# Kernel optimization log

Measured on AMD Instinct MI355X. Metric: run time of the kernel, lower is better.

Reference implementation:

```python
import jax, jax.numpy as jnp
import numpy as np

N_HEAD = 16

def setup_inputs() -> dict:
    key = jax.random.key(0)
    k0, k1, k2, k3 = jax.random.split(key, 4)
    S, E, H, T = 2048, 1024, N_HEAD, 4096
    d = E // H
    return {
        "x": jax.random.normal(k0, (S, E), jnp.float32),
        "past": jax.random.normal(k1, (2, H, T, d), jnp.float32),  # stacked [pk, pv]
        "W1": jax.random.normal(k2, (E, 3 * E), jnp.float32) * 0.02,  # c_attn (Conv1D k=1 == linear)
        "b1": jnp.zeros((3 * E,), jnp.float32),
        "W2": jax.random.normal(k3, (E, E), jnp.float32) * 0.02,  # c_proj
        "b2": jnp.zeros((E,), jnp.float32),
        "past_length": 2048,
    }


def reference(x, past, W1, b1, W2, b2, past_length):
    H = N_HEAD
    S, E = x.shape
    d = E // H

    c = x @ W1 + b1  # [S, 3E]
    q, k, v = jnp.split(c, 3, axis=1)

    def split_heads(t):  # [S, E] -> [H, S, d]
        return jnp.transpose(t.reshape(S, H, d), (1, 0, 2))

    q, k, v = split_heads(q), split_heads(k), split_heads(v)

    pk, pv = past[0], past[1]  # [H, T, d]
    k = jax.lax.dynamic_update_slice_in_dim(pk, k, past_length, axis=1)
    v = jax.lax.dynamic_update_slice_in_dim(pv, v, past_length, axis=1)

    # attention scores [H, S, T]
    w = jnp.einsum('hid,hjd->hij', q, k) / np.sqrt(d)
    ns = k.shape[1]
    i = jnp.arange(S)[:, None]
    j = jnp.arange(ns)[None, :]
    b = (i >= j - past_length).astype(w.dtype)
    w = w * b - jnp.float32(1e10) * (1 - b)
    w = jax.nn.softmax(w, axis=-1)

    a = jnp.einsum('hij,hjd->hid', w, v)  # [H, S, d]
    # faithful to original: start index clamps to 0 since axis len == S
    a = jax.lax.dynamic_slice_in_dim(a, past_length, S, axis=1)
    a = jnp.transpose(a, (1, 0, 2)).reshape(S, E)  # merge heads

    out = a @ W2 + b2
    new_cache = jnp.stack([k, v], axis=0)
    return out, new_cache
```

## Files before the change

### kernel.cpp

```cpp
#include <hip/hip_runtime.h>
#include <hip/hip_bf16.h>
#include <stdint.h>


#define S_LEN 2048
#define E_DIM 1024
#define NHEAD 16
#define HDIM  64
#define T_LEN 4096
#define PASTL 2048

typedef __bf16 bf16x8 __attribute__((ext_vector_type(8)));
typedef __bf16 bf16x4 __attribute__((ext_vector_type(4)));
typedef float  f32x4  __attribute__((ext_vector_type(4)));

static __device__ __forceinline__ f32x4 mfma_bf16(bf16x8 a, bf16x8 b, f32x4 c) {
  return __builtin_amdgcn_mfma_f32_16x16x32_bf16(a, b, c, 0, 0, 0);
}

static __device__ __forceinline__ unsigned int f2bf(float f) {
  union { float f; unsigned int u; } v; v.f = f;
  unsigned int u = v.u;
  return (u + 0x7fffu + ((u >> 16) & 1u)) >> 16;
}

static __device__ __forceinline__ float bf2f(unsigned short u) {
  union { unsigned int u; float f; } v; v.u = (unsigned int)u << 16;
  return v.f;
}

#define GLOBAL_LOAD_LDS16(gptr, lptr)                                              \
  __builtin_amdgcn_global_load_lds(                                                \
      (const __attribute__((address_space(1))) unsigned int*)(gptr),               \
      (__attribute__((address_space(3))) unsigned int*)(lptr), 16, 0, 0)

__global__ __launch_bounds__(256) void prep_kernel(
    const float* __restrict__ past, const float* __restrict__ x,
    const float* __restrict__ W1, const float* __restrict__ W2,
    float* __restrict__ cache, unsigned short* __restrict__ kb,
    unsigned short* __restrict__ xb, unsigned short* __restrict__ w1t,
    unsigned short* __restrict__ w2t, unsigned short* __restrict__ vtb) {
  __shared__ float tile[64][65];
  const int bid = blockIdx.x;
  const int tid = threadIdx.x;
  const int tx = tid & 63, ty = tid >> 6;

  if (bid < 512) {
    const int h = bid >> 5;
    const int t0 = (bid & 31) * 64;
    const float* in = past + (size_t)(NHEAD + h) * T_LEN * HDIM;
    unsigned short* outp = vtb + (size_t)h * HDIM * T_LEN;
#pragma unroll
    for (int r = 0; r < 64; r += 4)
      tile[r + ty][tx] = in[(size_t)(t0 + r + ty) * HDIM + tx];
    __syncthreads();
#pragma unroll
    for (int r = 0; r < 64; r += 4)
      outp[(size_t)(r + ty) * T_LEN + t0 + tx] = f2bf(tile[tx][r + ty]);
  } else if (bid < 1536) {
    const float* in;
    unsigned short* outp;
    int rows, cols, c0, r0;
    if (bid < 1280) {
      int u = bid - 512;
      in = W1; outp = w1t; rows = 1024; cols = 3072;
      c0 = (u % 48) * 64; r0 = (u / 48) * 64;
    } else {
      int u = bid - 1280;
      in = W2; outp = w2t; rows = 1024; cols = 1024;
      c0 = (u & 15) * 64; r0 = (u >> 4) * 64;
    }
#pragma unroll
    for (int r = 0; r < 64; r += 4)
      tile[r + ty][tx] = in[(size_t)(r0 + r + ty) * cols + c0 + tx];
    __syncthreads();
#pragma unroll
    for (int r = 0; r < 64; r += 4)
      outp[(size_t)(c0 + r + ty) * rows + r0 + tx] = f2bf(tile[tx][r + ty]);
  } else {
    const int n4p = (2 * NHEAD * PASTL * HDIM) / 4;
    const int n4x = (S_LEN * E_DIM) / 4;
    for (int i = (bid - 1536) * 256 + tid; i < n4p + n4x; i += 2048 * 256) {
      if (i < n4p) {
        int e = i * 4;
        int d = e & 63;
        int t = (e >> 6) & (PASTL - 1);
        int hh = (e >> 17) & (NHEAD - 1);
        int kv = e >> 21;
        size_t full = (((size_t)kv * NHEAD + hh) * T_LEN + t) * HDIM + d;
        float4 v = *(const float4*)(past + full);
        *(float4*)(cache + full) = v;
        if (kv == 0) {
          ushort4 u;
          u.x = f2bf(v.x); u.y = f2bf(v.y); u.z = f2bf(v.z); u.w = f2bf(v.w);
          *(ushort4*)(kb + full) = u;
        }
      } else {
        int j = i - n4p;
        float4 v = ((const float4*)x)[j];
        ushort4 u;
        u.x = f2bf(v.x); u.y = f2bf(v.y); u.z = f2bf(v.z); u.w = f2bf(v.w);
        ((ushort4*)xb)[j] = u;
      }
    }
  }
}

template <int MODE>
__global__ __launch_bounds__(256) void gemm_bt_kernel(
    const unsigned short* __restrict__ A, const unsigned short* __restrict__ Bt,
    const float* __restrict__ bias, int K,
    float* __restrict__ out_f32, unsigned short* __restrict__ qb,
    float* __restrict__ cache_k, float* __restrict__ cache_v,
    unsigned short* __restrict__ kb, unsigned short* __restrict__ vtb) {
  __shared__ alignas(16) unsigned short As[2][64 * 64];
  __shared__ alignas(16) unsigned short Bs[2][128 * 64];
  const int NPX = (MODE == 0) ? 3 : 1;
  const int bid = blockIdx.x;
  const int xcd = bid & 7;
  const int loc = bid >> 3;
  const int n_idx = xcd * NPX + loc % NPX;
  const int m_idx = loc / NPX;
  const int m0 = m_idx * 64, n0 = n_idx * 128;

  const int tid = threadIdx.x;
  const int lane = tid & 63;
  const int w = tid >> 6;
  const int wm = w >> 1, wn = w & 1;
  const int lr = lane & 15;
  const int lg = lane >> 4;

  f32x4 acc[2][4];
#pragma unroll
  for (int i = 0; i < 2; ++i)
#pragma unroll
    for (int j = 0; j < 4; ++j) acc[i][j] = f32x4{0.f, 0.f, 0.f, 0.f};

  const int srow = tid >> 3;
  const int sseg = (tid & 7) ^ (srow & 7);
  const unsigned short* ga0 = A + (size_t)(m0 + srow) * K + sseg * 8;
  const unsigned short* gb0 = Bt + (size_t)(n0 + srow) * K + sseg * 8;

  auto stage = [&](int b, int k0) {
    GLOBAL_LOAD_LDS16(ga0 + k0, (char*)As[b] + tid * 16);
    GLOBAL_LOAD_LDS16(ga0 + (size_t)32 * K + k0, (char*)As[b] + 4096 + tid * 16);
#pragma unroll
    for (int j = 0; j < 4; ++j)
      GLOBAL_LOAD_LDS16(gb0 + (size_t)(32 * j) * K + k0,
                        (char*)Bs[b] + j * 4096 + tid * 16);
  };

  const int NKS = K >> 6;
  stage(0, 0);
  int cur = 0;
  for (int i = 0; i < NKS; ++i) {
    asm volatile("s_waitcnt vmcnt(0)" ::: "memory");
    __builtin_amdgcn_s_barrier();
    __builtin_amdgcn_sched_barrier(0);
    if (i + 1 < NKS) stage(cur ^ 1, (i + 1) * 64);

#pragma unroll
    for (int kk = 0; kk < 2; ++kk) {
      bf16x8 af[2], bfr[4];
#pragma unroll
      for (int mi = 0; mi < 2; ++mi) {
        int row = wm * 32 + mi * 16 + lr;
        int slot = (kk * 4 + lg) ^ (row & 7);
        af[mi] = *reinterpret_cast<const bf16x8*>((const char*)As[cur] + row * 128 + slot * 16);
      }
#pragma unroll
      for (int ni = 0; ni < 4; ++ni) {
        int row = wn * 64 + ni * 16 + lr;
        int slot = (kk * 4 + lg) ^ (row & 7);
        bfr[ni] = *reinterpret_cast<const bf16x8*>((const char*)Bs[cur] + row * 128 + slot * 16);
      }
#pragma unroll
      for (int mi = 0; mi < 2; ++mi)
#pragma unroll
        for (int ni = 0; ni < 4; ++ni)
          acc[mi][ni] = mfma_bf16(af[mi], bfr[ni], acc[mi][ni]);
    }
    cur ^= 1;
  }

#pragma unroll
  for (int ni = 0; ni < 4; ++ni) {
    int n = n0 + wn * 64 + ni * 16 + lr;
    float bv = bias[n];
#pragma unroll
    for (int mi = 0; mi < 2; ++mi) {
      int mbase = m0 + wm * 32 + mi * 16 + lg * 4;
      float v4[4];
#pragma unroll
      for (int r = 0; r < 4; ++r) v4[r] = acc[mi][ni][r] + bv;
      if (MODE == 0) {
        if (n < E_DIM) {
#pragma unroll
          for (int r = 0; r < 4; ++r)
            qb[(size_t)(mbase + r) * E_DIM + n] = f2bf(v4[r] * 0.18033688f);
        } else if (n < 2 * E_DIM) {
          int e = n - E_DIM;
          size_t base = ((size_t)(e >> 6) * T_LEN + (PASTL + mbase)) * HDIM + (e & 63);
#pragma unroll
          for (int r = 0; r < 4; ++r) {
            cache_k[base + (size_t)r * HDIM] = v4[r];
            kb[base + (size_t)r * HDIM] = f2bf(v4[r]);
          }
        } else {
          int e = n - 2 * E_DIM;
          int hh = e >> 6, d = e & 63;
          size_t base = ((size_t)hh * T_LEN + (PASTL + mbase)) * HDIM + d;
#pragma unroll
          for (int r = 0; r < 4; ++r) cache_v[base + (size_t)r * HDIM] = v4[r];
          ushort4 u;
          u.x = f2bf(v4[0]); u.y = f2bf(v4[1]);
          u.z = f2bf(v4[2]); u.w = f2bf(v4[3]);
          *(ushort4*)(vtb + ((size_t)hh * HDIM + d) * T_LEN + PASTL + mbase) = u;
        }
      } else {
#pragma unroll
        for (int r = 0; r < 4; ++r)
          out_f32[(size_t)(mbase + r) * E_DIM + n] = v4[r];
      }
    }
  }
}

__global__ __launch_bounds__(256) void attn_kernel(
    const unsigned short* __restrict__ qb, const unsigned short* __restrict__ kb,
    const unsigned short* __restrict__ vt,
    unsigned short* __restrict__ o_part, float* __restrict__ l_part) {
  __shared__ alignas(16) unsigned short Ks[2][64 * 64];
  __shared__ alignas(16) unsigned short Vs[2][64 * 64];
  __shared__ alignas(16) __bf16 p_lds[4][32][72];
  const int fid = blockIdx.x;
  const int h = (fid & 7) + ((fid >= 448) ? 8 : 0);
  const int g = (fid >> 3) - ((fid >= 448) ? 56 : 0);
  int x, c;
  if (g < 24) { x = g / 3; c = g - 3 * x; }
  else { int g2 = g - 24; x = 8 + (g2 >> 2); c = g2 & 3; }

  const int tid = threadIdx.x;
  const int w = tid >> 6;
  const int lane = tid & 63;
  const int lr = lane & 15;
  const int lg = lane >> 4;
  const int qb0 = x * 128;
  const int q0 = qb0 + w * 32;

  const unsigned short* qr0 = qb + (size_t)(q0 + lr) * E_DIM + h * HDIM + lg * 8;
  const unsigned short* qr1 = qb + (size_t)(q0 + 16 + lr) * E_DIM + h * HDIM + lg * 8;
  const bf16x8 qf00 = *reinterpret_cast<const bf16x8*>(qr0);
  const bf16x8 qf01 = *reinterpret_cast<const bf16x8*>(qr0 + 32);
  const bf16x8 qf10 = *reinterpret_cast<const bf16x8*>(qr1);
  const bf16x8 qf11 = *reinterpret_cast<const bf16x8*>(qr1 + 32);

  const unsigned short* kh = kb + (size_t)h * T_LEN * HDIM;
  const unsigned short* vh = vt + (size_t)h * HDIM * T_LEN;

  const int srow = tid >> 3;
  const int sseg = (tid & 7) ^ (srow & 7);
  const unsigned short* ksrc = kh + (size_t)srow * HDIM + sseg * 8;
  const unsigned short* vsrc = vh + (size_t)srow * T_LEN + sseg * 8;

  f32x4 o[2][4];
  float lsum[2][2];
#pragma unroll
  for (int sb = 0; sb < 2; ++sb) {
    lsum[sb][0] = lsum[sb][1] = 0.f;
#pragma unroll
    for (int jd = 0; jd < 4; ++jd) o[sb][jd] = f32x4{0.f, 0.f, 0.f, 0.f};
  }

  const int jmaxq = q0 + PASTL;
  const int NTfull = 34 + 2 * x;
  const int tb = c * 16;
  const int te = (tb + 16 < NTfull) ? tb + 16 : NTfull;
  const int NT = te - tb;
  const int tbeg = tb * 64;

  auto stageK = [&](int b, int t0) {
    GLOBAL_LOAD_LDS16(ksrc + (size_t)t0 * HDIM, (char*)Ks[b] + tid * 16);
    GLOBAL_LOAD_LDS16(ksrc + (size_t)(t0 + 32) * HDIM, (char*)Ks[b] + 4096 + tid * 16);
  };
  auto stageV = [&](int b, int t0) {
    GLOBAL_LOAD_LDS16(vsrc + t0, (char*)Vs[b] + tid * 16);
    GLOBAL_LOAD_LDS16(vsrc + t0 + (size_t)32 * T_LEN, (char*)Vs[b] + 4096 + tid * 16);
  };

  stageK(0, tbeg);
  stageV(0, tbeg);
  int cur = 0;
  int t0 = tbeg;
  for (int i = 0; i < NT; ++i, t0 += 64) {
    const bool more = (i + 1 < NT);
    asm volatile("s_waitcnt vmcnt(2)" ::: "memory");
    __builtin_amdgcn_s_barrier();
    __builtin_amdgcn_sched_barrier(0);
    if (more) stageK(cur ^ 1, t0 + 64);

    bf16x8 kf[4][2];
#pragma unroll
    for (int j = 0; j < 4; ++j) {
      int row = j * 16 + lr;
      int s0 = lg ^ (row & 7), s1 = (4 + lg) ^ (row & 7);
      kf[j][0] = *reinterpret_cast<const bf16x8*>((const char*)Ks[cur] + row * 128 + s0 * 16);
      kf[j][1] = *reinterpret_cast<const bf16x8*>((const char*)Ks[cur] + row * 128 + s1 * 16);
    }

    f32x4 sc[2][4];
#pragma unroll
    for (int sb = 0; sb < 2; ++sb)
#pragma unroll
      for (int j = 0; j < 4; ++j) sc[sb][j] = f32x4{0.f, 0.f, 0.f, 0.f};
    __builtin_amdgcn_s_setprio(1);
#pragma unroll
    for (int j = 0; j < 4; ++j) {
      sc[0][j] = mfma_bf16(kf[j][0], qf00, sc[0][j]);
      sc[0][j] = mfma_bf16(kf[j][1], qf01, sc[0][j]);
      sc[1][j] = mfma_bf16(kf[j][0], qf10, sc[1][j]);
      sc[1][j] = mfma_bf16(kf[j][1], qf11, sc[1][j]);
    }
    __builtin_amdgcn_s_setprio(0);

    const bool partial = (t0 + 63 > jmaxq);
    const int thr = q0 + PASTL - t0 + lr;
    const int lg4 = lg * 4;
#pragma unroll
    for (int sb = 0; sb < 2; ++sb) {
#pragma unroll
      for (int j = 0; j < 4; ++j) {
        bf16x4 pk;
#pragma unroll
        for (int r = 0; r < 4; ++r) {
          float p = __builtin_amdgcn_exp2f(sc[sb][j][r]);
          if (partial && (j * 16 + lg4 + r > thr + sb * 16)) p = 0.f;
          lsum[sb][r >> 1] += p;
          pk[r] = (__bf16)p;
        }
        *reinterpret_cast<bf16x4*>(&p_lds[w][sb * 16 + lr][j * 16 + lg4]) = pk;
      }
    }
    bf16x8 pa[2][2];
#pragma unroll
    for (int sb = 0; sb < 2; ++sb) {
      pa[sb][0] = *reinterpret_cast<const bf16x8*>(&p_lds[w][sb * 16 + lr][lg * 8]);
      pa[sb][1] = *reinterpret_cast<const bf16x8*>(&p_lds[w][sb * 16 + lr][32 + lg * 8]);
    }

    if (more) {
      asm volatile("s_waitcnt vmcnt(2)" ::: "memory");
    } else {
      asm volatile("s_waitcnt vmcnt(0)" ::: "memory");
    }
    __builtin_amdgcn_s_barrier();
    __builtin_amdgcn_sched_barrier(0);
    if (more) stageV(cur ^ 1, t0 + 64);

    __builtin_amdgcn_s_setprio(1);
#pragma unroll
    for (int jd = 0; jd < 4; ++jd) {
      int row = jd * 16 + lr;
      int s0 = lg ^ (row & 7), s1 = (4 + lg) ^ (row & 7);
      bf16x8 vf0 = *reinterpret_cast<const bf16x8*>((const char*)Vs[cur] + row * 128 + s0 * 16);
      bf16x8 vf1 = *reinterpret_cast<const bf16x8*>((const char*)Vs[cur] + row * 128 + s1 * 16);
      o[0][jd] = mfma_bf16(pa[0][0], vf0, o[0][jd]);
      o[0][jd] = mfma_bf16(pa[0][1], vf1, o[0][jd]);
      o[1][jd] = mfma_bf16(pa[1][0], vf0, o[1][jd]);
      o[1][jd] = mfma_bf16(pa[1][1], vf1, o[1][jd]);
    }
    __builtin_amdgcn_s_setprio(0);
    cur ^= 1;
  }

  unsigned short* op = o_part + ((size_t)(c * NHEAD + h) * S_LEN) * HDIM;
  float* lp = l_part + (size_t)(c * NHEAD + h) * S_LEN;
#pragma unroll
  for (int sb = 0; sb < 2; ++sb) {
    float ls = lsum[sb][0] + lsum[sb][1];
    ls += __shfl_xor(ls, 16);
    ls += __shfl_xor(ls, 32);
    if (lg == 0) lp[q0 + sb * 16 + lr] = ls;
#pragma unroll
    for (int jd = 0; jd < 4; ++jd) {
#pragma unroll
      for (int r = 0; r < 4; ++r) {
        int row = q0 + sb * 16 + lg * 4 + r;
        op[(size_t)row * HDIM + jd * 16 + lr] = f2bf(o[sb][jd][r]);
      }
    }
  }
}

__global__ __launch_bounds__(256) void attn_merge_kernel(
    const unsigned short* __restrict__ o_part, const float* __restrict__ l_part,
    unsigned short* __restrict__ ab) {
  const int flat = blockIdx.x * 256 + threadIdx.x;
  const int d4 = flat & 15;
  const int row = (flat >> 4) & (S_LEN - 1);
  const int h = flat >> 15;
  const int nc = (row < 1024) ? 3 : 4;
  const size_t cstride_o = (size_t)NHEAD * S_LEN * HDIM;
  const size_t base_o = (((size_t)h * S_LEN) + row) * HDIM + d4 * 4;
  float acc[4] = {0.f, 0.f, 0.f, 0.f};
  float l = 0.f;
  for (int cc = 0; cc < nc; ++cc) {
    ushort4 u = *(const ushort4*)(o_part + cc * cstride_o + base_o);
    acc[0] += bf2f(u.x); acc[1] += bf2f(u.y);
    acc[2] += bf2f(u.z); acc[3] += bf2f(u.w);
    l += l_part[(size_t)cc * NHEAD * S_LEN + (size_t)h * S_LEN + row];
  }
  float inv = 1.f / l;
  ushort4 u;
  u.x = f2bf(acc[0] * inv);
  u.y = f2bf(acc[1] * inv);
  u.z = f2bf(acc[2] * inv);
  u.w = f2bf(acc[3] * inv);
  *(ushort4*)(ab + (size_t)row * E_DIM + h * HDIM + d4 * 4) = u;
}


extern "C" void kernel_launch(void* const* d_in, const int* in_sizes, int n_in,
                              void* d_out, int out_size, void* d_ws, size_t ws_size,
                              hipStream_t stream) {
  (void)in_sizes; (void)n_in; (void)out_size; (void)ws_size;
  const float* x    = (const float*)d_in[0];
  const float* past = (const float*)d_in[1];
  const float* W1   = (const float*)d_in[2];
  const float* b1   = (const float*)d_in[3];
  const float* W2   = (const float*)d_in[4];
  const float* b2   = (const float*)d_in[5];

  float* out = (float*)d_out;
  float* cache_k = out + (size_t)S_LEN * E_DIM;
  float* cache_v = cache_k + (size_t)NHEAD * T_LEN * HDIM;

  char* ws = (char*)d_ws;
  unsigned short* w2t = (unsigned short*)(ws);
  unsigned short* qb  = (unsigned short*)(ws + (size_t)(2u  << 20));
  unsigned short* kb  = (unsigned short*)(ws + (size_t)(6u  << 20));
  unsigned short* vtb = (unsigned short*)(ws + (size_t)(14u << 20));
  unsigned short* xb  = (unsigned short*)(ws + (size_t)(22u << 20));
  unsigned short* ab  = (unsigned short*)(ws + (size_t)(22u << 20));
  unsigned short* w1t = (unsigned short*)(ws + (size_t)(26u << 20));
  unsigned short* o_part = (unsigned short*)(ws + (size_t)(26u << 20));
  float* l_part = (float*)(ws + (size_t)(42u << 20));

  prep_kernel<<<3584, 256, 0, stream>>>(past, x, W1, W2, cache_k, kb, xb, w1t,
                                        w2t, vtb);
  gemm_bt_kernel<0><<<768, 256, 0, stream>>>(
      xb, w1t, b1, 1024, nullptr, qb, cache_k, cache_v, kb, vtb);
  attn_kernel<<<dim3(896), 256, 0, stream>>>(qb, kb, vtb, o_part, l_part);
  attn_merge_kernel<<<(NHEAD * S_LEN * 16) / 256, 256, 0, stream>>>(o_part, l_part, ab);
  gemm_bt_kernel<1><<<256, 256, 0, stream>>>(
      ab, w2t, b2, 1024, out, nullptr, nullptr, nullptr, nullptr, nullptr);
}
```

Baseline: 118.5 us.

## Switch attention to 32x32x16 MFMA and pass P via permlane32 swaps instead of LDS

Rewrites the attention inner loop to use 32x32x16 bf16 MFMA tiles so the transposed score layout lines up with the PV operand layout. The probabilities are packed to bf16 pairs in registers and rearranged across half-waves with permlane32_swap, which removes the per-tile LDS round trip through p_lds. Unmasked tiles also get a branch-free exp path. This changes the register layout and the output write pattern, and the larger accumulators may add register pressure.

```diff
diff --git a/kernel.cpp b/kernel.cpp
--- a/kernel.cpp
+++ b/kernel.cpp
@@ -12,10 +12,16 @@
 
 typedef __bf16 bf16x8 __attribute__((ext_vector_type(8)));
 typedef __bf16 bf16x4 __attribute__((ext_vector_type(4)));
+typedef __bf16 bf16x2 __attribute__((ext_vector_type(2)));
 typedef float  f32x4  __attribute__((ext_vector_type(4)));
+typedef float  f32x16 __attribute__((ext_vector_type(16)));
+typedef unsigned u32x2 __attribute__((ext_vector_type(2)));
 
 static __device__ __forceinline__ f32x4 mfma_bf16(bf16x8 a, bf16x8 b, f32x4 c) {
   return __builtin_amdgcn_mfma_f32_16x16x32_bf16(a, b, c, 0, 0, 0);
+}
+static __device__ __forceinline__ f32x16 mfma32(bf16x8 a, bf16x8 b, f32x16 c) {
+  return __builtin_amdgcn_mfma_f32_32x32x16_bf16(a, b, c, 0, 0, 0);
 }
 
 static __device__ __forceinline__ unsigned int f2bf(float f) {
@@ -27,6 +33,11 @@
 static __device__ __forceinline__ float bf2f(unsigned short u) {
   union { unsigned int u; float f; } v; v.u = (unsigned int)u << 16;
   return v.f;
+}
+
+static __device__ __forceinline__ unsigned pkbf(float lo, float hi) {
+  bf16x2 t = {(__bf16)lo, (__bf16)hi};
+  return __builtin_bit_cast(unsigned, t);
 }
 
 #define GLOBAL_LOAD_LDS16(gptr, lptr)                                              \
@@ -232,7 +243,6 @@
     unsigned short* __restrict__ o_part, float* __restrict__ l_part) {
   __shared__ alignas(16) unsigned short Ks[2][64 * 64];
   __shared__ alignas(16) unsigned short Vs[2][64 * 64];
-  __shared__ alignas(16) __bf16 p_lds[4][32][72];
   const int fid = blockIdx.x;
   const int h = (fid & 7) + ((fid >= 448) ? 8 : 0);
   const int g = (fid >> 3) - ((fid >= 448) ? 56 : 0);
@@ -243,17 +253,16 @@
   const int tid = threadIdx.x;
   const int w = tid >> 6;
   const int lane = tid & 63;
-  const int lr = lane & 15;
-  const int lg = lane >> 4;
-  const int qb0 = x * 128;
-  const int q0 = qb0 + w * 32;
-
-  const unsigned short* qr0 = qb + (size_t)(q0 + lr) * E_DIM + h * HDIM + lg * 8;
-  const unsigned short* qr1 = qb + (size_t)(q0 + 16 + lr) * E_DIM + h * HDIM + lg * 8;
-  const bf16x8 qf00 = *reinterpret_cast<const bf16x8*>(qr0);
-  const bf16x8 qf01 = *reinterpret_cast<const bf16x8*>(qr0 + 32);
-  const bf16x8 qf10 = *reinterpret_cast<const bf16x8*>(qr1);
-  const bf16x8 qf11 = *reinterpret_cast<const bf16x8*>(qr1 + 32);
+  const int l31 = lane & 31;
+  const int hi = lane >> 5;
+  const int hi4 = hi * 4;
+  const int q0 = x * 128 + w * 32;
+
+  const unsigned short* qrow = qb + (size_t)(q0 + l31) * E_DIM + h * HDIM + hi * 8;
+  bf16x8 qf[4];
+#pragma unroll
+  for (int kk = 0; kk < 4; ++kk)
+    qf[kk] = *reinterpret_cast<const bf16x8*>(qrow + kk * 16);
 
   const unsigned short* kh = kb + (size_t)h * T_LEN * HDIM;
   const unsigned short* vh = vt + (size_t)h * HDIM * T_LEN;
@@ -263,21 +272,17 @@
   const unsigned short* ksrc = kh + (size_t)srow * HDIM + sseg * 8;
   const unsigned short* vsrc = vh + (size_t)srow * T_LEN + sseg * 8;
 
-  f32x4 o[2][4];
-  float lsum[2][2];
-#pragma unroll
-  for (int sb = 0; sb < 2; ++sb) {
-    lsum[sb][0] = lsum[sb][1] = 0.f;
-#pragma unroll
-    for (int jd = 0; jd < 4; ++jd) o[sb][jd] = f32x4{0.f, 0.f, 0.f, 0.f};
-  }
-
-  const int jmaxq = q0 + PASTL;
+  f32x16 o0, o1, zc;
+#pragma unroll
+  for (int i = 0; i < 16; ++i) { o0[i] = 0.f; o1[i] = 0.f; zc[i] = 0.f; }
+  float lsum = 0.f;
+
   const int NTfull = 34 + 2 * x;
   const int tb = c * 16;
   const int te = (tb + 16 < NTfull) ? tb + 16 : NTfull;
   const int NT = te - tb;
   const int tbeg = tb * 64;
+  const int qpp = q0 + l31 + PASTL;
 
   auto stageK = [&](int b, int t0) {
     GLOBAL_LOAD_LDS16(ksrc + (size_t)t0 * HDIM, (char*)Ks[b] + tid * 16);
@@ -299,53 +304,73 @@
     __builtin_amdgcn_sched_barrier(0);
     if (more) stageK(cur ^ 1, t0 + 64);
 
-    bf16x8 kf[4][2];
-#pragma unroll
-    for (int j = 0; j < 4; ++j) {
-      int row = j * 16 + lr;
-      int s0 = lg ^ (row & 7), s1 = (4 + lg) ^ (row & 7);
-      kf[j][0] = *reinterpret_cast<const bf16x8*>((const char*)Ks[cur] + row * 128 + s0 * 16);
-      kf[j][1] = *reinterpret_cast<const bf16x8*>((const char*)Ks[cur] + row * 128 + s1 * 16);
-    }
-
-    f32x4 sc[2][4];
-#pragma unroll
-    for (int sb = 0; sb < 2; ++sb)
-#pragma unroll
-      for (int j = 0; j < 4; ++j) sc[sb][j] = f32x4{0.f, 0.f, 0.f, 0.f};
+    f32x16 s0, s1;
     __builtin_amdgcn_s_setprio(1);
-#pragma unroll
-    for (int j = 0; j < 4; ++j) {
-      sc[0][j] = mfma_bf16(kf[j][0], qf00, sc[0][j]);
-      sc[0][j] = mfma_bf16(kf[j][1], qf01, sc[0][j]);
-      sc[1][j] = mfma_bf16(kf[j][0], qf10, sc[1][j]);
-      sc[1][j] = mfma_bf16(kf[j][1], qf11, sc[1][j]);
+    {
+      int sl = hi ^ (l31 & 7);
+      bf16x8 k0 = *reinterpret_cast<const bf16x8*>((const char*)Ks[cur] + l31 * 128 + sl * 16);
+      bf16x8 k1 = *reinterpret_cast<const bf16x8*>((const char*)Ks[cur] + (32 + l31) * 128 + sl * 16);
+      s0 = mfma32(k0, qf[0], zc);
+      s1 = mfma32(k1, qf[0], zc);
+    }
+#pragma unroll
+    for (int kk = 1; kk < 4; ++kk) {
+      int sl = (kk * 2 + hi) ^ (l31 & 7);
+      bf16x8 k0 = *reinterpret_cast<const bf16x8*>((const char*)Ks[cur] + l31 * 128 + sl * 16);
+      bf16x8 k1 = *reinterpret_cast<const bf16x8*>((const char*)Ks[cur] + (32 + l31) * 128 + sl * 16);
+      s0 = mfma32(k0, qf[kk], s0);
+      s1 = mfma32(k1, qf[kk], s1);
     }
     __builtin_amdgcn_s_setprio(0);
 
-    const bool partial = (t0 + 63 > jmaxq);
-    const int thr = q0 + PASTL - t0 + lr;
-    const int lg4 = lg * 4;
-#pragma unroll
-    for (int sb = 0; sb < 2; ++sb) {
-#pragma unroll
-      for (int j = 0; j < 4; ++j) {
-        bf16x4 pk;
-#pragma unroll
-        for (int r = 0; r < 4; ++r) {
-          float p = __builtin_amdgcn_exp2f(sc[sb][j][r]);
-          if (partial && (j * 16 + lg4 + r > thr + sb * 16)) p = 0.f;
-          lsum[sb][r >> 1] += p;
-          pk[r] = (__bf16)p;
-        }
-        *reinterpret_cast<bf16x4*>(&p_lds[w][sb * 16 + lr][j * 16 + lg4]) = pk;
-      }
-    }
-    bf16x8 pa[2][2];
-#pragma unroll
-    for (int sb = 0; sb < 2; ++sb) {
-      pa[sb][0] = *reinterpret_cast<const bf16x8*>(&p_lds[w][sb * 16 + lr][lg * 8]);
-      pa[sb][1] = *reinterpret_cast<const bf16x8*>(&p_lds[w][sb * 16 + lr][32 + lg * 8]);
+    const bool partial = (t0 + 63 > q0 + PASTL);
+    unsigned aw[8], bw[8];
+    if (!partial) {
+#pragma unroll
+      for (int i2 = 0; i2 < 8; ++i2) {
+        float p0 = __builtin_amdgcn_exp2f(s0[2 * i2]);
+        float p1 = __builtin_amdgcn_exp2f(s0[2 * i2 + 1]);
+        float p2 = __builtin_amdgcn_exp2f(s1[2 * i2]);
+        float p3 = __builtin_amdgcn_exp2f(s1[2 * i2 + 1]);
+        lsum += (p0 + p1) + (p2 + p3);
+        aw[i2] = pkbf(p0, p1);
+        bw[i2] = pkbf(p2, p3);
+      }
+    } else {
+      const int thr = qpp - t0;
+#pragma unroll
+      for (int i2 = 0; i2 < 8; ++i2) {
+        int r0 = 2 * i2;
+        int ko = (r0 & 3) + 8 * (r0 >> 2) + hi4;
+        float p0 = __builtin_amdgcn_exp2f(s0[r0]);
+        float p1 = __builtin_amdgcn_exp2f(s0[r0 + 1]);
+        float p2 = __builtin_amdgcn_exp2f(s1[r0]);
+        float p3 = __builtin_amdgcn_exp2f(s1[r0 + 1]);
+        if (ko > thr) p0 = 0.f;
+        if (ko + 1 > thr) p1 = 0.f;
+        if (ko + 32 > thr) p2 = 0.f;
+        if (ko + 33 > thr) p3 = 0.f;
+        lsum += (p0 + p1) + (p2 + p3);
+        aw[i2] = pkbf(p0, p1);
+        bw[i2] = pkbf(p2, p3);
+      }
+    }
+
+    union U4 { unsigned u[4]; bf16x8 v; };
+    U4 pa0, pa1, pa2, pa3;
+    {
+      u32x2 r02 = __builtin_amdgcn_permlane32_swap(aw[0], aw[2], false, false);
+      u32x2 r13 = __builtin_amdgcn_permlane32_swap(aw[1], aw[3], false, false);
+      pa0.u[0] = r02[0]; pa0.u[1] = r13[0]; pa0.u[2] = r02[1]; pa0.u[3] = r13[1];
+      u32x2 r46 = __builtin_amdgcn_permlane32_swap(aw[4], aw[6], false, false);
+      u32x2 r57 = __builtin_amdgcn_permlane32_swap(aw[5], aw[7], false, false);
+      pa1.u[0] = r46[0]; pa1.u[1] = r57[0]; pa1.u[2] = r46[1]; pa1.u[3] = r57[1];
+      u32x2 s02 = __builtin_amdgcn_permlane32_swap(bw[0], bw[2], false, false);
+      u32x2 s13 = __builtin_amdgcn_permlane32_swap(bw[1], bw[3], false, false);
+      pa2.u[0] = s02[0]; pa2.u[1] = s13[0]; pa2.u[2] = s02[1]; pa2.u[3] = s13[1];
+      u32x2 s46 = __builtin_amdgcn_permlane32_swap(bw[4], bw[6], false, false);
+      u32x2 s57 = __builtin_amdgcn_permlane32_swap(bw[5], bw[7], false, false);
+      pa3.u[0] = s46[0]; pa3.u[1] = s57[0]; pa3.u[2] = s46[1]; pa3.u[3] = s57[1];
     }
 
     if (more) {
@@ -358,37 +383,48 @@
     if (more) stageV(cur ^ 1, t0 + 64);
 
     __builtin_amdgcn_s_setprio(1);
-#pragma unroll
-    for (int jd = 0; jd < 4; ++jd) {
-      int row = jd * 16 + lr;
-      int s0 = lg ^ (row & 7), s1 = (4 + lg) ^ (row & 7);
-      bf16x8 vf0 = *reinterpret_cast<const bf16x8*>((const char*)Vs[cur] + row * 128 + s0 * 16);
-      bf16x8 vf1 = *reinterpret_cast<const bf16x8*>((const char*)Vs[cur] + row * 128 + s1 * 16);
-      o[0][jd] = mfma_bf16(pa[0][0], vf0, o[0][jd]);
-      o[0][jd] = mfma_bf16(pa[0][1], vf1, o[0][jd]);
-      o[1][jd] = mfma_bf16(pa[1][0], vf0, o[1][jd]);
-      o[1][jd] = mfma_bf16(pa[1][1], vf1, o[1][jd]);
+    {
+      int sl = hi ^ (l31 & 7);
+      bf16x8 v0 = *reinterpret_cast<const bf16x8*>((const char*)Vs[cur] + l31 * 128 + sl * 16);
+      bf16x8 v1 = *reinterpret_cast<const bf16x8*>((const char*)Vs[cur] + (32 + l31) * 128 + sl * 16);
+      o0 = mfma32(pa0.v, v0, o0);
+      o1 = mfma32(pa0.v, v1, o1);
+    }
+    {
+      int sl = (2 + hi) ^ (l31 & 7);
+      bf16x8 v0 = *reinterpret_cast<const bf16x8*>((const char*)Vs[cur] + l31 * 128 + sl * 16);
+      bf16x8 v1 = *reinterpret_cast<const bf16x8*>((const char*)Vs[cur] + (32 + l31) * 128 + sl * 16);
+      o0 = mfma32(pa1.v, v0, o0);
+      o1 = mfma32(pa1.v, v1, o1);
+    }
+    {
+      int sl = (4 + hi) ^ (l31 & 7);
+      bf16x8 v0 = *reinterpret_cast<const bf16x8*>((const char*)Vs[cur] + l31 * 128 + sl * 16);
+      bf16x8 v1 = *reinterpret_cast<const bf16x8*>((const char*)Vs[cur] + (32 + l31) * 128 + sl * 16);
+      o0 = mfma32(pa2.v, v0, o0);
+      o1 = mfma32(pa2.v, v1, o1);
+    }
+    {
+      int sl = (6 + hi) ^ (l31 & 7);
+      bf16x8 v0 = *reinterpret_cast<const bf16x8*>((const char*)Vs[cur] + l31 * 128 + sl * 16);
+      bf16x8 v1 = *reinterpret_cast<const bf16x8*>((const char*)Vs[cur] + (32 + l31) * 128 + sl * 16);
+      o0 = mfma32(pa3.v, v0, o0);
+      o1 = mfma32(pa3.v, v1, o1);
     }
     __builtin_amdgcn_s_setprio(0);
     cur ^= 1;
   }
 
+  lsum += __shfl_xor(lsum, 32);
+
   unsigned short* op = o_part + ((size_t)(c * NHEAD + h) * S_LEN) * HDIM;
   float* lp = l_part + (size_t)(c * NHEAD + h) * S_LEN;
-#pragma unroll
-  for (int sb = 0; sb < 2; ++sb) {
-    float ls = lsum[sb][0] + lsum[sb][1];
-    ls += __shfl_xor(ls, 16);
-    ls += __shfl_xor(ls, 32);
-    if (lg == 0) lp[q0 + sb * 16 + lr] = ls;
-#pragma unroll
-    for (int jd = 0; jd < 4; ++jd) {
-#pragma unroll
-      for (int r = 0; r < 4; ++r) {
-        int row = q0 + sb * 16 + lg * 4 + r;
-        op[(size_t)row * HDIM + jd * 16 + lr] = f2bf(o[sb][jd][r]);
-      }
-    }
+  if (hi == 0) lp[q0 + l31] = lsum;
+#pragma unroll
+  for (int r = 0; r < 16; ++r) {
+    int qr = (r & 3) + 8 * (r >> 2) + hi4;
+    op[(size_t)(q0 + qr) * HDIM + l31] = f2bf(o0[r]);
+    op[(size_t)(q0 + qr) * HDIM + 32 + l31] = f2bf(o1[r]);
   }
 }
 
```

Measured after the change: 118.9 us. Within noise of the previous version (+0.4%).
